# Kernel tuning notes

Measured on AMD Instinct MI355X. Metric: run time of the kernel, lower is better.

Reference implementation:

```python
import jax, jax.numpy as jnp
import numpy as np

B = 512          # batch of graphs
N_LOCAL = 33     # local nodes per graph
NPG = 34         # nodes per graph (1 global + 33 local)
C = 768          # feat_dims[-1] (global feature channels)
FEAT = 1152      # concat_dim = sum(feat_dims) = 384 + 768
GPD = 2048       # global_proj_dim
HID = 1024       # hidden_dim_proj
H = 8            # num_heads
AD = 64          # att_dim
LLM = 4096       # llama_dim
DEG = 8          # average degree of random graph
E_PER = NPG * DEG
NT = B * NPG     # total nodes


def setup_inputs() -> dict:
    key = jax.random.key(0)
    ks = jax.random.split(key, 16)
    sc = 0.02
    local_features = jax.random.normal(ks[0], (B, 1, N_LOCAL, FEAT), jnp.float32)
    global_features = jax.random.normal(ks[1], (B, C, 8, 8, 4), jnp.float32)
    # random batched graph: edges stay within each graph, offset by 34*b
    src = jax.random.randint(ks[2], (B, E_PER), 0, NPG)
    dst = jax.random.randint(ks[3], (B, E_PER), 0, NPG)
    off = (jnp.arange(B, dtype=jnp.int32) * NPG)[:, None]
    edge_index = jnp.stack([(src + off).reshape(-1), (dst + off).reshape(-1)]).astype(jnp.int32)
    return {
        "local_features": local_features,
        "global_features": global_features,
        "edge_index": edge_index,
        "W1g": jax.random.normal(ks[4], (32 * C, GPD), jnp.float32) * sc,
        "b1g": jnp.zeros((GPD,), jnp.float32),
        "W2g": jax.random.normal(ks[5], (GPD, FEAT), jnp.float32) * sc,
        "b2g": jnp.zeros((FEAT,), jnp.float32),
        "Wp": jax.random.normal(ks[6], (FEAT, HID), jnp.float32) * sc,
        "bp": jnp.zeros((HID,), jnp.float32),
        "Wg": jax.random.normal(ks[7], (HID, H * AD), jnp.float32) * sc,
        "a_src": jax.random.normal(ks[8], (H, AD), jnp.float32) * sc,
        "a_dst": jax.random.normal(ks[9], (H, AD), jnp.float32) * sc,
        "Wllm": jax.random.normal(ks[10], (H * AD, LLM), jnp.float32) * sc,
        "bllm": jnp.zeros((LLM,), jnp.float32),
    }


def reference(local_features, global_features, edge_index,
              W1g, b1g, W2g, b2g, Wp, bp, Wg, a_src, a_dst, Wllm, bllm):
    # AdaptiveAvgPool3d((4,4,2)) on (8,8,4): exact 2x2x2 mean pooling
    x = global_features.reshape(B, C, 4, 2, 4, 2, 2, 2).mean(axis=(3, 5, 7))
    x = x.reshape(B, -1)                                   # [B, 32*C]
    out_global = jax.nn.relu(x @ W1g + b1g) @ W2g + b2g    # [B, FEAT]
    # concat global node with local nodes -> [B, 34, FEAT] -> flatten batched graph
    nodes = jnp.concatenate([out_global[:, None, :], local_features[:, 0]], axis=1)
    nodes = nodes.reshape(NT, FEAT)

    # GAT layer: hidden projection, per-head features, edge attention
    h = jax.nn.relu(nodes @ Wp + bp)                       # [NT, HID]
    z = (h @ Wg).reshape(NT, H, AD)                        # [NT, H, AD]
    s, d = edge_index[0], edge_index[1]
    e = jax.nn.leaky_relu(
        jnp.einsum('ehd,hd->eh', z[s], a_src) + jnp.einsum('ehd,hd->eh', z[d], a_dst),
        negative_slope=0.2)                                # [E, H]
    m = jax.ops.segment_max(e, d, num_segments=NT)
    m = jnp.where(jnp.isfinite(m), m, 0.0)                 # guard isolated nodes
    ex = jnp.exp(e - m[d])
    den = jax.ops.segment_sum(ex, d, num_segments=NT)
    alpha = ex / (den[d] + 1e-9)                           # neighbor softmax per dst
    agg = jax.ops.segment_sum(alpha[:, :, None] * z[s], d, num_segments=NT)  # [NT, H, AD]
    gnn_feats = agg.reshape(NT, H * AD)

    out = gnn_feats.reshape(B, NPG, H * AD) @ Wllm + bllm  # [B, 34, LLM]
    return out
```

## Files before the change

### kernel.cpp

```cpp
#include <hip/hip_runtime.h>
#include <hip/hip_bf16.h>
#include <math.h>

#define BB    512
#define NPG   34
#define NT    17408
#define FEAT  1152
#define GPD   2048
#define HID   1024
#define NH    8
#define AD    64
#define HA    512
#define LLM   4096
#define EPG   272
#define NE    139264
#define C32   24576
#define CC    768

#define AS3 __attribute__((address_space(3)))
#define AS1 __attribute__((address_space(1)))

typedef __attribute__((ext_vector_type(8))) short short8v;
typedef __attribute__((ext_vector_type(4))) float f32x4;

__device__ __forceinline__ ushort f2bf(float f) {
    __hip_bfloat16 h = __float2bfloat16(f);
    return __builtin_bit_cast(ushort, h);
}

__device__ __forceinline__ void d_transpose(const float* __restrict__ W, ushort* __restrict__ WT,
                                            int R, int Cn, int bx, int by,
                                            float (*tile)[33], int tid) {
    int c0 = bx * 32, r0 = by * 32;
    int tc = tid & 31, tr = tid >> 5;
#pragma unroll
    for (int i = 0; i < 4; i++)
        tile[tr + i * 8][tc] = W[(size_t)(r0 + tr + i * 8) * Cn + c0 + tc];
    __syncthreads();
#pragma unroll
    for (int it = 0; it < 2; it++) {
        int p = tid + it * 256;
        int c = p >> 4, pr = (p & 15) << 1;
        ushort2 v;
        v.x = f2bf(tile[pr][c]);
        v.y = f2bf(tile[pr + 1][c]);
        *(ushort2*)&WT[(size_t)(c0 + c) * R + r0 + pr] = v;
    }
}

__device__ __forceinline__ void d_pool(const float* __restrict__ gf, ushort* __restrict__ outB,
                                       int blk, int tid) {
    int t = blk * 256 + tid;
    int q = t & 15; int bc = t >> 4;
    int dO = q >> 2, hO = q & 3;
    const float* p = gf + (size_t)bc * 256 + dO * 64 + hO * 8;
    float4 r00 = *(const float4*)(p);
    float4 r01 = *(const float4*)(p + 4);
    float4 r10 = *(const float4*)(p + 32);
    float4 r11 = *(const float4*)(p + 36);
    float o0 = (r00.x + r00.y + r01.x + r01.y + r10.x + r10.y + r11.x + r11.y) * 0.125f;
    float o1 = (r00.z + r00.w + r01.z + r01.w + r10.z + r10.w + r11.z + r11.w) * 0.125f;
    int b = bc / CC, c = bc % CC;
    ushort2 v; v.x = f2bf(o0); v.y = f2bf(o1);
    *(ushort2*)(outB + (size_t)b * C32 + c * 32 + dO * 8 + hO * 2) = v;
}

__global__ __launch_bounds__(256) void k_prep(
    const float* __restrict__ W1g, ushort* __restrict__ W1gT,
    const float* __restrict__ W2g, ushort* __restrict__ W2gT,
    const float* __restrict__ Wp,  ushort* __restrict__ WpT,
    const float* __restrict__ Wg,  ushort* __restrict__ WgT,
    const float* __restrict__ Wllm, ushort* __restrict__ WllmT,
    const float* __restrict__ gf,  ushort* __restrict__ poolB) {
    __shared__ float tile[32][33];
    int blk = blockIdx.x, tid = threadIdx.x;
    if (blk < 49152) {
        d_transpose(W1g, W1gT, C32, GPD, blk & 63, blk >> 6, tile, tid);
    } else if (blk < 51456) {
        int l = blk - 49152; d_transpose(W2g, W2gT, GPD, FEAT, l % 36, l / 36, tile, tid);
    } else if (blk < 52608) {
        int l = blk - 51456; d_transpose(Wp, WpT, FEAT, HID, l & 31, l >> 5, tile, tid);
    } else if (blk < 53120) {
        int l = blk - 52608; d_transpose(Wg, WgT, HID, HA, l & 15, l >> 4, tile, tid);
    } else if (blk < 55168) {
        int l = blk - 53120; d_transpose(Wllm, WllmT, HA, LLM, l & 127, l >> 7, tile, tid);
    } else {
        d_pool(gf, poolB, blk - 55168, tid);
    }
}

#define GLDS(gp, lp) __builtin_amdgcn_global_load_lds((const AS1 void*)(gp), (AS3 void*)(lp), 16, 0, 0)
#define STAGE_A(buf, h, tt) { \
    const ushort* s_ = gAs + (size_t)(tt) * 64 + (size_t)(2 * (h)) * rK; \
    ushort* d_ = lds + (buf) * 32768 + (2 * (h)) * 4096 + (w << 9); \
    GLDS(s_, d_); GLDS(s_ + rK, d_ + 4096); }
#define STAGE_B(buf, h, tt) { \
    const ushort* s_ = gBs + (size_t)(tt) * 64 + (size_t)(2 * (h)) * rK; \
    ushort* d_ = lds + (buf) * 32768 + 16384 + (2 * (h)) * 4096 + (w << 9); \
    GLDS(s_, d_); GLDS(s_ + rK, d_ + 4096); }
#define DSRA(BO, mh) { _Pragma("unroll") for (int mf = 0; mf < 4; mf++) { \
    const ushort* p_ = lds + (BO) + aBase + ((mh) * 64 + mf * 16) * 64; \
    aF[mf][0] = *(const short8v*)(p_ + k0s); \
    aF[mf][1] = *(const short8v*)(p_ + k1s); } }
#define DSRB(BO, nh, BF) { _Pragma("unroll") for (int nf = 0; nf < 2; nf++) { \
    const ushort* p_ = lds + (BO) + bBase + ((nh) * 32 + nf * 16) * 64; \
    BF[nf][0] = *(const short8v*)(p_ + k0s); \
    BF[nf][1] = *(const short8v*)(p_ + k1s); } }
#define MM(mh, nh, BF) { \
    asm volatile("s_waitcnt lgkmcnt(0)" ::: "memory"); \
    __builtin_amdgcn_sched_barrier(0); \
    __builtin_amdgcn_s_setprio(1); \
    _Pragma("unroll") for (int mf = 0; mf < 4; mf++) \
    _Pragma("unroll") for (int nf = 0; nf < 2; nf++) { \
        acc[(mh)*4+mf][(nh)*2+nf] = __builtin_amdgcn_mfma_f32_16x16x32_bf16(aF[mf][0], BF[nf][0], acc[(mh)*4+mf][(nh)*2+nf], 0, 0, 0); \
        acc[(mh)*4+mf][(nh)*2+nf] = __builtin_amdgcn_mfma_f32_16x16x32_bf16(aF[mf][1], BF[nf][1], acc[(mh)*4+mf][(nh)*2+nf], 0, 0, 0); } \
    __builtin_amdgcn_s_setprio(0); }
#define BAR __builtin_amdgcn_s_barrier()
#define VMW4 { asm volatile("s_waitcnt vmcnt(4)" ::: "memory"); __builtin_amdgcn_sched_barrier(0); }

template<bool SPLITK, bool BIAS, bool RELU, bool OUTBF>
__global__ __launch_bounds__(512, 2) void k_gemm256(
    const ushort* __restrict__ A, const ushort* __restrict__ BT,
    const float* __restrict__ bias, void* __restrict__ Cout,
    int M, int N, int K, int kChunk) {
    __shared__ ushort lds[65536];
    const int t = threadIdx.x;
    const int w = t >> 6, l = t & 63;
    const int wm = w >> 2, wn = w & 3;
    const int gx = gridDim.x;
    const int nwg = gx * gridDim.y;
    const int id = blockIdx.y * gx + blockIdx.x;
    const int qx = nwg >> 3, rx = nwg & 7;
    const int xcd = id & 7, pos = id >> 3;
    const int nid = (xcd < rx ? xcd * (qx + 1) : rx * (qx + 1) + (xcd - rx) * qx) + pos;
    const int m0 = (nid / gx) * 256, n0 = (nid % gx) * 256;
    const int kBase = SPLITK ? blockIdx.z * kChunk : 0;
    const int NTt = (SPLITK ? kChunk : K) / 64;

    const int rowLo = t >> 3;
    const int keSrc = ((t & 7) << 3) ^ (((rowLo >> 2) & 1) << 5) ^ (((rowLo >> 3) & 1) << 4);
    const ushort* gAs = A + (size_t)(m0 + rowLo) * K + kBase + keSrc;
    const ushort* gBs = BT + (size_t)(n0 + rowLo) * K + kBase + keSrc;
    const size_t rK = (size_t)64 * K;

    const int fcol = l & 15, fk = (l >> 4) << 3;
    const int flipR = (((l >> 2) & 1) << 5) | (((l >> 3) & 1) << 4);
    const int k0s = fk ^ flipR;
    const int k1s = fk ^ 32 ^ flipR;
    const int aBase = (wm * 128 + fcol) * 64;
    const int bBase = 16384 + (wn * 64 + fcol) * 64;

    short8v aF[4][2], bF0[2][2], bF1[2][2];
    f32x4 acc[8][4] = {};

    STAGE_B(0, 0, 0); STAGE_B(0, 1, 0); STAGE_A(0, 0, 0); STAGE_A(0, 1, 0);
    STAGE_B(1, 0, 1); STAGE_B(1, 1, 1);
    VMW4;
    BAR;

    const int NITER = NTt >> 1;
    for (int it = 0; it < NITER; ++it) {
        const int t1 = 2 * it + 1;
        const int t2r = 2 * it + 2, t3r = 2 * it + 3;
        const int t2 = t2r < NTt ? t2r : 0;
        const int t3 = t3r < NTt ? t3r : 0;
        DSRA(0, 0); DSRB(0, 0, bF0); STAGE_A(1, 0, t1);
        BAR; MM(0, 0, bF0); BAR;
        DSRB(0, 1, bF1); STAGE_A(1, 1, t1);
        BAR; MM(0, 1, bF1); BAR;
        DSRA(0, 1); STAGE_B(0, 0, t2);
        BAR; MM(1, 1, bF1); BAR;
        STAGE_B(0, 1, t2); VMW4;
        BAR; MM(1, 0, bF0); BAR;
        DSRA(32768, 0); DSRB(32768, 0, bF0); STAGE_A(0, 0, t2);
        BAR; MM(0, 0, bF0); BAR;
        DSRB(32768, 1, bF1); STAGE_A(0, 1, t2);
        BAR; MM(0, 1, bF1); BAR;
        DSRA(32768, 1); STAGE_B(1, 0, t3);
        BAR; MM(1, 1, bF1); BAR;
        STAGE_B(1, 1, t3); VMW4;
        BAR; MM(1, 0, bF0); BAR;
    }
    asm volatile("s_waitcnt vmcnt(0)" ::: "memory");
    BAR;

    const int orow = (l >> 4) << 2;
    float* eph = ((float*)lds) + w * 2176;
    const int ecol = (l & 15) << 2;
    const int erow4 = l >> 4;
#pragma unroll
    for (int pass = 0; pass < 4; pass++) {
#pragma unroll
        for (int mi = 0; mi < 2; mi++) {
            int mf = pass * 2 + mi;
#pragma unroll
            for (int nf = 0; nf < 4; nf++)
#pragma unroll
                for (int r = 0; r < 4; r++)
                    eph[(mi * 16 + orow + r) * 68 + nf * 16 + fcol] = acc[mf][nf][r];
        }
#pragma unroll
        for (int g = 0; g < 8; g++) {
            int lrow = g * 4 + erow4;
            f32x4 v = *(f32x4*)&eph[lrow * 68 + ecol];
            int row = m0 + wm * 128 + pass * 32 + lrow;
            int col = n0 + wn * 64 + ecol;
            if (BIAS) {
                float4 bb = *(const float4*)(bias + col);
                v[0] += bb.x; v[1] += bb.y; v[2] += bb.z; v[3] += bb.w;
            }
            if (RELU) {
#pragma unroll
                for (int q = 0; q < 4; q++) v[q] = v[q] > 0.f ? v[q] : 0.f;
            }
            if (OUTBF) {
                ushort4 u;
                u.x = f2bf(v[0]); u.y = f2bf(v[1]); u.z = f2bf(v[2]); u.w = f2bf(v[3]);
                *(ushort4*)&((ushort*)Cout)[(size_t)row * N + col] = u;
            } else {
                size_t off = (size_t)row * N + col;
                if (SPLITK) off += (size_t)blockIdx.z * (size_t)M * N;
                float4 fv = {v[0], v[1], v[2], v[3]};
                *(float4*)&((float*)Cout)[off] = fv;
            }
        }
    }
}

template<bool SPLITK, bool BIAS, bool RELU, bool OUTBF>
__global__ __launch_bounds__(256) void k_gemm_bf(
    const ushort* __restrict__ A, const ushort* __restrict__ BT,
    const float* __restrict__ bias, void* __restrict__ Cout,
    int M, int N, int K, int kChunk) {
    __shared__ ushort lA[128 * 32];
    __shared__ ushort lB[128 * 32];
    const int t = threadIdx.x;
    const int w = t >> 6, l = t & 63;
    const int m0 = blockIdx.y * 128, n0 = blockIdx.x * 128;
    const int kLen = SPLITK ? kChunk : K;
    const int k0 = SPLITK ? blockIdx.z * kChunk : 0;
    const int srow = w * 16 + (l >> 2);
    const int skq = (l & 3) << 3;
    const ushort* gA = A + (size_t)(m0 + srow) * K + k0 + skq;
    const ushort* gB = BT + (size_t)(n0 + srow) * K + k0 + skq;
    ushort* lA0 = lA + w * 512;
    ushort* lB0 = lB + w * 512;
    const size_t str64 = (size_t)64 * K;
    const int wr = (w >> 1) << 6, wc = (w & 1) << 6;
    const int fcol = l & 15, fk = (l >> 4) << 3;

    f32x4 acc[4][4] = {};
    for (int kk = 0; kk < kLen; kk += 32) {
        __syncthreads();
        GLDS(gA + kk,         lA0);
        GLDS(gA + kk + str64, lA0 + 2048);
        GLDS(gB + kk,         lB0);
        GLDS(gB + kk + str64, lB0 + 2048);
        __syncthreads();
        short8v a[4], b[4];
#pragma unroll
        for (int f = 0; f < 4; f++) {
            a[f] = *(const short8v*)(lA + (wr + f * 16 + fcol) * 32 + fk);
            b[f] = *(const short8v*)(lB + (wc + f * 16 + fcol) * 32 + fk);
        }
#pragma unroll
        for (int i = 0; i < 4; i++)
#pragma unroll
            for (int j = 0; j < 4; j++)
                acc[i][j] = __builtin_amdgcn_mfma_f32_16x16x32_bf16(a[i], b[j], acc[i][j], 0, 0, 0);
    }
    const int orow = (l >> 4) << 2;
#pragma unroll
    for (int i = 0; i < 4; i++) {
#pragma unroll
        for (int j = 0; j < 4; j++) {
            int col = n0 + wc + j * 16 + fcol;
            float bv = BIAS ? bias[col] : 0.f;
#pragma unroll
            for (int r = 0; r < 4; r++) {
                int row = m0 + wr + i * 16 + orow + r;
                float v = acc[i][j][r] + bv;
                if (RELU) v = v > 0.f ? v : 0.f;
                if (OUTBF) {
                    ((ushort*)Cout)[(size_t)row * N + col] = f2bf(v);
                } else {
                    size_t off = (size_t)row * N + col;
                    if (SPLITK) off += (size_t)blockIdx.z * (size_t)M * N;
                    ((float*)Cout)[off] = v;
                }
            }
        }
    }
}

template<int NP, bool RELU>
__global__ __launch_bounds__(256) void k_red(const float* __restrict__ part,
                                             const float* __restrict__ bias,
                                             ushort* __restrict__ outB,
                                             int N, int stride) {
    int i = blockIdx.x * 256 + threadIdx.x;
    float s = bias[i % N];
#pragma unroll
    for (int q = 0; q < NP; q++) s += part[i + (size_t)q * stride];
    if (RELU) s = s > 0.f ? s : 0.f;
    outB[i] = f2bf(s);
}

__global__ __launch_bounds__(256) void k_nodes(const ushort* __restrict__ outgB,
                                               const float* __restrict__ locf,
                                               ushort* __restrict__ nodesB) {
    int idx = blockIdx.x * 256 + threadIdx.x;
    int node = idx / 144, cc = idx - node * 144;
    int b = node / NPG, j = node - b * NPG;
    int c = cc * 8;
    ushort* dst = nodesB + (size_t)node * FEAT + c;
    if (j == 0) {
        *(uint4*)dst = *(const uint4*)(outgB + (size_t)b * FEAT + c);
    } else {
        const float* s = locf + ((size_t)b * 33 + (j - 1)) * FEAT + c;
        float4 v0 = *(const float4*)s, v1 = *(const float4*)(s + 4);
        ushort u[8] = {f2bf(v0.x), f2bf(v0.y), f2bf(v0.z), f2bf(v0.w),
                       f2bf(v1.x), f2bf(v1.y), f2bf(v1.z), f2bf(v1.w)};
        *(uint4*)dst = *(uint4*)u;
    }
}

__global__ __launch_bounds__(512) void k_gat(const int* __restrict__ es, const int* __restrict__ ed,
                                             const float* __restrict__ z,
                                             const float* __restrict__ a_src,
                                             const float* __restrict__ a_dst,
                                             ushort* __restrict__ gnnB) {
    __shared__ float zt[NPG][520];
    __shared__ float sps[NPG][NH], spd[NPG][NH], sm[NPG][NH], sden[NPG][NH];
    __shared__ float esc[EPG][NH];
    __shared__ int srcl[EPG], dll[EPG], order[EPG], cnt[NPG], bstart[NPG + 1];
    int b = blockIdx.x, t = threadIdx.x;
    for (int i = t; i < NPG * 128; i += 512) {
        int n = i >> 7, c4 = (i & 127) << 2;
        *(float4*)&zt[n][c4] = *(const float4*)&z[((size_t)b * NPG + n) * HA + c4];
    }
    for (int e = t; e < EPG; e += 512) {
        srcl[e] = es[b * EPG + e] - b * NPG;
        dll[e]  = ed[b * EPG + e] - b * NPG;
    }
    if (t < NPG) cnt[t] = 0;
    __syncthreads();
    {
        int wv = t >> 6, l = t & 63;
        for (int n = wv; n < NPG; n += 8) {
            float s[NH], d[NH];
#pragma unroll
            for (int i = 0; i < NH; i++) {
                float zv = zt[n][i * 64 + l];
                s[i] = zv * a_src[i * 64 + l];
                d[i] = zv * a_dst[i * 64 + l];
            }
#pragma unroll
            for (int i = 0; i < NH; i++) {
#pragma unroll
                for (int off = 32; off > 0; off >>= 1) {
                    s[i] += __shfl_xor(s[i], off);
                    d[i] += __shfl_xor(d[i], off);
                }
            }
            if (l == 0) {
#pragma unroll
                for (int i = 0; i < NH; i++) { sps[n][i] = s[i]; spd[n][i] = d[i]; }
            }
        }
    }
    for (int e = t; e < EPG; e += 512) atomicAdd(&cnt[dll[e]], 1);
    __syncthreads();
    if (t == 0) {
        int s = 0;
        for (int n = 0; n < NPG; n++) { bstart[n] = s; s += cnt[n]; cnt[n] = bstart[n]; }
        bstart[NPG] = s;
        for (int e = 0; e < EPG; e++) order[cnt[dll[e]]++] = e;
    }
    __syncthreads();
    for (int i = t; i < EPG * NH; i += 512) {
        int e = i >> 3, h = i & 7;
        float sc = sps[srcl[e]][h] + spd[dll[e]][h];
        esc[e][h] = sc > 0.f ? sc : 0.2f * sc;
    }
    __syncthreads();
    for (int i = t; i < NPG * NH; i += 512) {
        int n = i >> 3, h = i & 7;
        float m = -INFINITY;
        for (int j = bstart[n]; j < bstart[n + 1]; j++) m = fmaxf(m, esc[order[j]][h]);
        if (m == -INFINITY) m = 0.f;
        float den = 0.f;
        for (int j = bstart[n]; j < bstart[n + 1]; j++) den += expf(esc[order[j]][h] - m);
        sm[n][h] = m; sden[n][h] = den;
    }
    __syncthreads();
    for (int i = t; i < EPG * NH; i += 512) {
        int e = i >> 3, h = i & 7;
        esc[e][h] = expf(esc[e][h] - sm[dll[e]][h]) / (sden[dll[e]][h] + 1e-9f);
    }
    __syncthreads();
    for (int c = t; c < NPG * 64; c += 512) {
        int n = c >> 6, rem = c & 63, h = rem >> 3, d0 = (rem & 7) << 3;
        float acc[8] = {};
        for (int j = bstart[n]; j < bstart[n + 1]; j++) {
            int e = order[j];
            float a = esc[e][h];
            const float* zp = &zt[srcl[e]][h * 64 + d0];
#pragma unroll
            for (int q = 0; q < 8; q++) acc[q] = fmaf(a, zp[q], acc[q]);
        }
        ushort u[8];
#pragma unroll
        for (int q = 0; q < 8; q++) u[q] = f2bf(acc[q]);
        *(uint4*)&gnnB[((size_t)b * NPG + n) * HA + h * 64 + d0] = *(uint4*)u;
    }
}

extern "C" void kernel_launch(void* const* d_in, const int* in_sizes, int n_in,
                              void* d_out, int out_size, void* d_ws, size_t ws_size,
                              hipStream_t stream) {
    const float* locf  = (const float*)d_in[0];
    const float* gf    = (const float*)d_in[1];
    const int*   ei    = (const int*)d_in[2];
    const float* W1g   = (const float*)d_in[3];
    const float* b1g   = (const float*)d_in[4];
    const float* W2g   = (const float*)d_in[5];
    const float* b2g   = (const float*)d_in[6];
    const float* Wp    = (const float*)d_in[7];
    const float* bp    = (const float*)d_in[8];
    const float* Wg    = (const float*)d_in[9];
    const float* a_src = (const float*)d_in[10];
    const float* a_dst = (const float*)d_in[11];
    const float* Wllm  = (const float*)d_in[12];
    const float* bllm  = (const float*)d_in[13];
    float* out = (float*)d_out;
    float* ws  = (float*)d_ws;
    const int* es = ei;
    const int* ed = ei + NE;

    float*  z      = out;
    ushort* W1gT   = (ushort*)(out + 8912896);
    ushort* hB     = (ushort*)(out + 8912896);
    ushort* poolB  = (ushort*)(out + 34078720);
    float*  part1  = out + 40370176;
    ushort* nodesB = (ushort*)(out + 40370176);
    ushort* g1B    = (ushort*)(out + 57147392);
    ushort* W2gT   = (ushort*)(out + 57671680);
    ushort* WpT    = (ushort*)(out + 58851328);
    ushort* WgT    = (ushort*)(out + 59441152);
    ushort* outgB  = (ushort*)(out + 59703296);
    float*  part2  = out + 59998208;
    ushort* WllmT = (ushort*)ws;
    ushort* gnnB  = (ushort*)(ws + 1048576);

    k_prep<<<79744, 256, 0, stream>>>(W1g, W1gT, W2g, W2gT, Wp, WpT, Wg, WgT,
                                      Wllm, WllmT, gf, poolB);
    k_gemm256<true, false, false, false><<<dim3(8, 2, 16), 512, 0, stream>>>(
        poolB, W1gT, nullptr, part1, 512, GPD, C32, 1536);
    k_red<16, true><<<4096, 256, 0, stream>>>(part1, b1g, g1B, GPD, 1048576);
    k_gemm_bf<true, false, false, false><<<dim3(9, 4, 4), 256, 0, stream>>>(
        g1B, W2gT, nullptr, part2, 512, FEAT, GPD, 512);
    k_red<4, false><<<2304, 256, 0, stream>>>(part2, b2g, outgB, FEAT, 589824);
    k_nodes<<<9792, 256, 0, stream>>>(outgB, locf, nodesB);
    k_gemm256<false, true, true, true><<<dim3(4, 68), 512, 0, stream>>>(
        nodesB, WpT, bp, hB, NT, HID, FEAT, 0);
    k_gemm256<false, false, false, false><<<dim3(2, 68), 512, 0, stream>>>(
        hB, WgT, nullptr, z, NT, HA, HID, 0);
    k_gat<<<BB, 512, 0, stream>>>(es, ed, z, a_src, a_dst, gnnB);
    k_gemm256<false, true, false, false><<<dim3(16, 68), 512, 0, stream>>>(
        gnnB, WllmT, bllm, out, NT, LLM, HA, 0);
}
```

Measured before the change: 575.7 us.

## Widen weight transpose tiles, store split-K partials in bf16, fuse reductions into consumers

The weight transpose moves from 32x32 to 64x64 tiles, so each thread writes 16-byte bf16 chunks instead of 4-byte pairs and far fewer blocks are launched. The first split-K GEMM now writes its partials as bf16 rather than fp32, halving that traffic, and a vectorized reduction kernel sums them. The second split-K reduction is folded into the node-assembly kernel, which removes one launch and one intermediate buffer. Summing bf16 partials costs some precision in the 16-way reduction.

```diff
diff --git a/kernel.cpp b/kernel.cpp
--- a/kernel.cpp
+++ b/kernel.cpp
@@ -27,24 +27,30 @@
     __hip_bfloat16 h = __float2bfloat16(f);
     return __builtin_bit_cast(ushort, h);
 }
-
-__device__ __forceinline__ void d_transpose(const float* __restrict__ W, ushort* __restrict__ WT,
-                                            int R, int Cn, int bx, int by,
-                                            float (*tile)[33], int tid) {
-    int c0 = bx * 32, r0 = by * 32;
-    int tc = tid & 31, tr = tid >> 5;
-#pragma unroll
-    for (int i = 0; i < 4; i++)
-        tile[tr + i * 8][tc] = W[(size_t)(r0 + tr + i * 8) * Cn + c0 + tc];
-    __syncthreads();
-#pragma unroll
-    for (int it = 0; it < 2; it++) {
-        int p = tid + it * 256;
-        int c = p >> 4, pr = (p & 15) << 1;
-        ushort2 v;
-        v.x = f2bf(tile[pr][c]);
-        v.y = f2bf(tile[pr + 1][c]);
-        *(ushort2*)&WT[(size_t)(c0 + c) * R + r0 + pr] = v;
+__device__ __forceinline__ float bf2f(ushort u) {
+    unsigned int x = ((unsigned int)u) << 16;
+    return __builtin_bit_cast(float, x);
+}
+
+__device__ __forceinline__ void d_transpose64(const float* __restrict__ W, ushort* __restrict__ WT,
+                                              int R, int Cn, int bx, int by,
+                                              float (*tile)[65], int tid) {
+    int c0 = bx * 64, r0 = by * 64;
+    int rc = tid >> 6, cc = tid & 63;
+#pragma unroll
+    for (int i = 0; i < 16; i++) {
+        int r = i * 4 + rc;
+        tile[r][cc] = W[(size_t)(r0 + r) * Cn + c0 + cc];
+    }
+    __syncthreads();
+#pragma unroll
+    for (int i = 0; i < 2; i++) {
+        int p = tid + i * 256;
+        int c = p >> 3, ro = (p & 7) << 3;
+        ushort u[8];
+#pragma unroll
+        for (int k = 0; k < 8; k++) u[k] = f2bf(tile[ro + k][c]);
+        *(uint4*)&WT[(size_t)(c0 + c) * R + r0 + ro] = *(uint4*)u;
     }
 }
 
@@ -72,20 +78,20 @@
     const float* __restrict__ Wg,  ushort* __restrict__ WgT,
     const float* __restrict__ Wllm, ushort* __restrict__ WllmT,
     const float* __restrict__ gf,  ushort* __restrict__ poolB) {
-    __shared__ float tile[32][33];
+    __shared__ float tile[64][65];
     int blk = blockIdx.x, tid = threadIdx.x;
-    if (blk < 49152) {
-        d_transpose(W1g, W1gT, C32, GPD, blk & 63, blk >> 6, tile, tid);
-    } else if (blk < 51456) {
-        int l = blk - 49152; d_transpose(W2g, W2gT, GPD, FEAT, l % 36, l / 36, tile, tid);
-    } else if (blk < 52608) {
-        int l = blk - 51456; d_transpose(Wp, WpT, FEAT, HID, l & 31, l >> 5, tile, tid);
-    } else if (blk < 53120) {
-        int l = blk - 52608; d_transpose(Wg, WgT, HID, HA, l & 15, l >> 4, tile, tid);
-    } else if (blk < 55168) {
-        int l = blk - 53120; d_transpose(Wllm, WllmT, HA, LLM, l & 127, l >> 7, tile, tid);
+    if (blk < 12288) {
+        d_transpose64(W1g, W1gT, C32, GPD, blk & 31, blk >> 5, tile, tid);
+    } else if (blk < 12864) {
+        int l = blk - 12288; d_transpose64(W2g, W2gT, GPD, FEAT, l % 18, l / 18, tile, tid);
+    } else if (blk < 13152) {
+        int l = blk - 12864; d_transpose64(Wp, WpT, FEAT, HID, l & 15, l >> 4, tile, tid);
+    } else if (blk < 13280) {
+        int l = blk - 13152; d_transpose64(Wg, WgT, HID, HA, l & 7, l >> 3, tile, tid);
+    } else if (blk < 13792) {
+        int l = blk - 13280; d_transpose64(Wllm, WllmT, HA, LLM, l & 63, l >> 6, tile, tid);
     } else {
-        d_pool(gf, poolB, blk - 55168, tid);
+        d_pool(gf, poolB, blk - 13792, tid);
     }
 }
 
@@ -213,13 +219,13 @@
 #pragma unroll
                 for (int q = 0; q < 4; q++) v[q] = v[q] > 0.f ? v[q] : 0.f;
             }
+            size_t off = (size_t)row * N + col;
+            if (SPLITK) off += (size_t)blockIdx.z * (size_t)M * N;
             if (OUTBF) {
                 ushort4 u;
                 u.x = f2bf(v[0]); u.y = f2bf(v[1]); u.z = f2bf(v[2]); u.w = f2bf(v[3]);
-                *(ushort4*)&((ushort*)Cout)[(size_t)row * N + col] = u;
+                *(ushort4*)&((ushort*)Cout)[off] = u;
             } else {
-                size_t off = (size_t)row * N + col;
-                if (SPLITK) off += (size_t)blockIdx.z * (size_t)M * N;
                 float4 fv = {v[0], v[1], v[2], v[3]};
                 *(float4*)&((float*)Cout)[off] = fv;
             }
@@ -293,20 +299,28 @@
     }
 }
 
-template<int NP, bool RELU>
-__global__ __launch_bounds__(256) void k_red(const float* __restrict__ part,
-                                             const float* __restrict__ bias,
-                                             ushort* __restrict__ outB,
-                                             int N, int stride) {
-    int i = blockIdx.x * 256 + threadIdx.x;
-    float s = bias[i % N];
-#pragma unroll
-    for (int q = 0; q < NP; q++) s += part[i + (size_t)q * stride];
-    if (RELU) s = s > 0.f ? s : 0.f;
-    outB[i] = f2bf(s);
-}
-
-__global__ __launch_bounds__(256) void k_nodes(const ushort* __restrict__ outgB,
+__global__ __launch_bounds__(256) void k_red1(const ushort* __restrict__ part,
+                                              const float* __restrict__ b1g,
+                                              ushort* __restrict__ g1B) {
+    int i8 = (blockIdx.x * 256 + threadIdx.x) * 8;
+    float v[8];
+#pragma unroll
+    for (int k = 0; k < 8; k++) v[k] = b1g[(i8 + k) & (GPD - 1)];
+#pragma unroll
+    for (int q = 0; q < 16; q++) {
+        uint4 pk = *(const uint4*)(part + (size_t)q * 1048576 + i8);
+        const ushort* pu = (const ushort*)&pk;
+#pragma unroll
+        for (int k = 0; k < 8; k++) v[k] += bf2f(pu[k]);
+    }
+    ushort u[8];
+#pragma unroll
+    for (int k = 0; k < 8; k++) u[k] = f2bf(v[k] > 0.f ? v[k] : 0.f);
+    *(uint4*)&g1B[i8] = *(uint4*)u;
+}
+
+__global__ __launch_bounds__(256) void k_nodes(const float* __restrict__ part2,
+                                               const float* __restrict__ b2g,
                                                const float* __restrict__ locf,
                                                ushort* __restrict__ nodesB) {
     int idx = blockIdx.x * 256 + threadIdx.x;
@@ -315,7 +329,21 @@
     int c = cc * 8;
     ushort* dst = nodesB + (size_t)node * FEAT + c;
     if (j == 0) {
-        *(uint4*)dst = *(const uint4*)(outgB + (size_t)b * FEAT + c);
+        float v[8];
+        float4 b0 = *(const float4*)(b2g + c), b1 = *(const float4*)(b2g + c + 4);
+        v[0] = b0.x; v[1] = b0.y; v[2] = b0.z; v[3] = b0.w;
+        v[4] = b1.x; v[5] = b1.y; v[6] = b1.z; v[7] = b1.w;
+#pragma unroll
+        for (int q = 0; q < 4; q++) {
+            const float* pp = part2 + (size_t)q * 589824 + (size_t)b * FEAT + c;
+            float4 p0 = *(const float4*)pp, p1 = *(const float4*)(pp + 4);
+            v[0] += p0.x; v[1] += p0.y; v[2] += p0.z; v[3] += p0.w;
+            v[4] += p1.x; v[5] += p1.y; v[6] += p1.z; v[7] += p1.w;
+        }
+        ushort u[8];
+#pragma unroll
+        for (int k = 0; k < 8; k++) u[k] = f2bf(v[k]);
+        *(uint4*)dst = *(uint4*)u;
     } else {
         const float* s = locf + ((size_t)b * 33 + (j - 1)) * FEAT + c;
         float4 v0 = *(const float4*)s, v1 = *(const float4*)(s + 4);
@@ -442,26 +470,24 @@
     ushort* W1gT   = (ushort*)(out + 8912896);
     ushort* hB     = (ushort*)(out + 8912896);
     ushort* poolB  = (ushort*)(out + 34078720);
-    float*  part1  = out + 40370176;
+    ushort* part1B = (ushort*)(out + 40370176);
     ushort* nodesB = (ushort*)(out + 40370176);
     ushort* g1B    = (ushort*)(out + 57147392);
     ushort* W2gT   = (ushort*)(out + 57671680);
     ushort* WpT    = (ushort*)(out + 58851328);
     ushort* WgT    = (ushort*)(out + 59441152);
-    ushort* outgB  = (ushort*)(out + 59703296);
     float*  part2  = out + 59998208;
     ushort* WllmT = (ushort*)ws;
     ushort* gnnB  = (ushort*)(ws + 1048576);
 
-    k_prep<<<79744, 256, 0, stream>>>(W1g, W1gT, W2g, W2gT, Wp, WpT, Wg, WgT,
+    k_prep<<<38368, 256, 0, stream>>>(W1g, W1gT, W2g, W2gT, Wp, WpT, Wg, WgT,
                                       Wllm, WllmT, gf, poolB);
-    k_gemm256<true, false, false, false><<<dim3(8, 2, 16), 512, 0, stream>>>(
-        poolB, W1gT, nullptr, part1, 512, GPD, C32, 1536);
-    k_red<16, true><<<4096, 256, 0, stream>>>(part1, b1g, g1B, GPD, 1048576);
+    k_gemm256<true, false, false, true><<<dim3(8, 2, 16), 512, 0, stream>>>(
+        poolB, W1gT, nullptr, part1B, 512, GPD, C32, 1536);
+    k_red1<<<512, 256, 0, stream>>>(part1B, b1g, g1B);
     k_gemm_bf<true, false, false, false><<<dim3(9, 4, 4), 256, 0, stream>>>(
         g1B, W2gT, nullptr, part2, 512, FEAT, GPD, 512);
-    k_red<4, false><<<2304, 256, 0, stream>>>(part2, b2g, outgB, FEAT, 589824);
-    k_nodes<<<9792, 256, 0, stream>>>(outgB, locf, nodesB);
+    k_nodes<<<9792, 256, 0, stream>>>(part2, b2g, locf, nodesB);
     k_gemm256<false, true, true, true><<<dim3(4, 68), 512, 0, stream>>>(
         nodesB, WpT, bp, hB, NT, HID, FEAT, 0);
     k_gemm256<false, false, false, false><<<dim3(2, 68), 512, 0, stream>>>(
```

Result: faster. 554.3 us (-3.7%).
